# Kernel tuning notes

Measured on AMD Instinct MI355X. Metric: run time of the kernel, lower is better.

Reference implementation:

```python
import jax, jax.numpy as jnp
import numpy as np

D = 2048      # hidden_size
W = 4         # kernel_size
DG = 2048     # generator hidden size (no reduction)

def setup_inputs() -> dict:
    key = jax.random.key(0)
    k1, k2, k3, k4 = jax.random.split(key, 4)
    x = jax.random.normal(k1, (2, 4096, D), dtype=jnp.float32)
    # Linear weights stored torch-style [out, in]; scaled small for sane activations
    w1 = jax.random.normal(k2, (DG, D), dtype=jnp.float32) * 0.02
    w2 = jax.random.normal(k3, (D * W, DG), dtype=jnp.float32) * 0.02
    b2 = jax.random.normal(k4, (D * W,), dtype=jnp.float32) * 0.02
    return {"x": x, "w1": w1, "w2": w2, "b2": b2}

def reference(x, w1, w2, b2):
    B, T, Dh = x.shape
    # kernel generator: w2(silu(w1 @ x)) + b2 -> per-position kernels [B,T,D,W]
    h = jax.nn.silu(jnp.einsum('btd,gd->btg', x, w1))
    flat = jnp.einsum('btg,kg->btk', h, w2) + b2
    kernels = flat.reshape(B, T, Dh, W)
    # causal depthwise dynamic conv: y[b,t,d] = sum_w x[b, t-(W-1)+w, d] * k[b,t,d,w]
    xp = jnp.pad(x, ((0, 0), (W - 1, 0), (0, 0)))
    y = xp[:, 0:T, :] * kernels[..., 0]
    for w in range(1, W):  # small fixed-width loop over kernel taps
        y = y + xp[:, w:w + T, :] * kernels[..., w]
    return jax.nn.silu(y)
```

## Files before the change

kernel.cpp:

```cpp
#include <hip/hip_runtime.h>
#include <cstdint>

#define D_DIM  2048
#define T_DIM  4096
#define B_DIM  2
#define M_DIM  8192
#define DG_DIM 2048
#define N2_DIM 8192
#define K_DIM  2048
#define NT_TILES (K_DIM / 64)

typedef __bf16 bf16x8 __attribute__((ext_vector_type(8)));
typedef __bf16 bf16x4 __attribute__((ext_vector_type(4)));
typedef float  f32x4  __attribute__((ext_vector_type(4)));

__device__ __forceinline__ void gload_lds16(const void* g, void* l) {
  __builtin_amdgcn_global_load_lds(
      (__attribute__((address_space(1))) void*)g,
      (__attribute__((address_space(3))) void*)l, 16, 0, 0);
}

__device__ __forceinline__ float silu_f(float a) {
  return a / (1.f + __expf(-a));
}

__global__ void cast_f32_bf16(const float* __restrict__ src,
                              __bf16* __restrict__ dst, int n4) {
  int i = blockIdx.x * blockDim.x + threadIdx.x;
  if (i >= n4) return;
  float4 v = ((const float4*)src)[i];
  bf16x4 o;
  o[0] = (__bf16)v.x; o[1] = (__bf16)v.y; o[2] = (__bf16)v.z; o[3] = (__bf16)v.w;
  ((bf16x4*)dst)[i] = o;
}

__global__ void cast_permute_w2(const float* __restrict__ src,
                                __bf16* __restrict__ dst, int n4) {
  int i = blockIdx.x * blockDim.x + threadIdx.x;
  if (i >= n4) return;
  const int row = i >> 9;
  const int pos = i & 511;
  const int blk = row >> 8;
  const int cw  = row & 255;
  const int j   = cw >> 6;
  const int wn  = (cw >> 4) & 3;
  const int ln  = cw & 15;
  const int d   = blk * 64 + wn * 16 + ln;
  const int k   = 4 * d + j;
  float4 v = ((const float4*)src)[(size_t)k * 512 + pos];
  bf16x4 o;
  o[0] = (__bf16)v.x; o[1] = (__bf16)v.y; o[2] = (__bf16)v.z; o[3] = (__bf16)v.w;
  ((bf16x4*)dst)[i] = o;
}


__device__ __forceinline__ void stage_unit(const __bf16* src, __bf16* sX,
                                           int s, int hf, int lq0) {
  const int k0 = (s < NT_TILES) ? (s * 64) : 0;
  __bf16* dst = sX + ((s & 1) * 2 + hf) * 8192;
  const size_t goff = (size_t)hf * 128 * K_DIM + k0;
  gload_lds16(src + goff, dst + lq0);
  gload_lds16(src + goff + (size_t)64 * K_DIM, dst + lq0 + 4096);
}

__device__ __forceinline__ void read4(bf16x8 dst[4][2], const __bf16* base,
                                      const int off[4][2]) {
#pragma unroll
  for (int i = 0; i < 4; i++) {
    dst[i][0] = *(const bf16x8*)(base + off[i][0]);
    dst[i][1] = *(const bf16x8*)(base + off[i][1]);
  }
}

__device__ __forceinline__ void read2(bf16x8 dst[2][2], const __bf16* base,
                                      const int off[2][2]) {
#pragma unroll
  for (int j = 0; j < 2; j++) {
    dst[j][0] = *(const bf16x8*)(base + off[j][0]);
    dst[j][1] = *(const bf16x8*)(base + off[j][1]);
  }
}

__device__ __forceinline__ void mmaq(f32x4 acc[8][4], int ib, int jb,
                                     const bf16x8 a[4][2], const bf16x8 b[2][2]) {
  __builtin_amdgcn_s_setprio(1);
#pragma unroll
  for (int kk = 0; kk < 2; kk++)
#pragma unroll
    for (int i = 0; i < 4; i++)
#pragma unroll
      for (int j = 0; j < 2; j++)
        acc[ib + i][jb + j] = __builtin_amdgcn_mfma_f32_16x16x32_bf16(
            a[i][kk], b[j][kk], acc[ib + i][jb + j], 0, 0, 0);
  __builtin_amdgcn_s_setprio(0);
}

__device__ __forceinline__ void body_fn(f32x4 acc[8][4],
    bf16x8 aL[4][2], bf16x8 aH[4][2], bf16x8 b0[2][2], bf16x8 b1[2][2],
    const __bf16* nA, const __bf16* nB,
    const __bf16* a_src, const __bf16* b_src,
    __bf16* sA, __bf16* sB, int s2, int lq0,
    const int aoff[4][2], const int boff[2][2]) {
  mmaq(acc, 0, 0, aL, b0);
  __builtin_amdgcn_sched_barrier(0);
  stage_unit(a_src, sA, s2, 0, lq0);
  stage_unit(a_src, sA, s2, 1, lq0);
  stage_unit(b_src, sB, s2, 0, lq0);
  stage_unit(b_src, sB, s2, 1, lq0);
  __builtin_amdgcn_sched_barrier(0);
  mmaq(acc, 4, 0, aH, b0);
  __builtin_amdgcn_sched_barrier(0);
  read2(b0, nB, boff);
  __builtin_amdgcn_sched_barrier(0);
  mmaq(acc, 4, 2, aH, b1);
  __builtin_amdgcn_sched_barrier(0);
  read4(aH, nA + 8192, aoff);
  __builtin_amdgcn_sched_barrier(0);
  __builtin_amdgcn_s_setprio(1);
#pragma unroll
  for (int i = 0; i < 4; i++) {
#pragma unroll
    for (int kk = 0; kk < 2; kk++)
#pragma unroll
      for (int j = 0; j < 2; j++)
        acc[i][2 + j] = __builtin_amdgcn_mfma_f32_16x16x32_bf16(
            aL[i][kk], b1[j][kk], acc[i][2 + j], 0, 0, 0);
    aL[i][0] = *(const bf16x8*)(nA + aoff[i][0]);
    aL[i][1] = *(const bf16x8*)(nA + aoff[i][1]);
  }
  __builtin_amdgcn_s_setprio(0);
  __builtin_amdgcn_sched_barrier(0);
  read2(b1, nB + 8192, boff);
  asm volatile("s_waitcnt lgkmcnt(0)" ::: "memory");
  asm volatile("s_waitcnt vmcnt(0)" ::: "memory");
  __builtin_amdgcn_sched_barrier(0);
  __builtin_amdgcn_s_barrier();
  __builtin_amdgcn_sched_barrier(0);
}

__device__ __forceinline__ void gemm_core(const __bf16* __restrict__ A,
                                          const __bf16* __restrict__ B,
                                          int m0, int n0,
                                          __bf16* sA, __bf16* sB,
                                          f32x4 acc[8][4]) {
  constexpr int K = K_DIM;
  const int t    = threadIdx.x;
  const int lane = t & 63;
  const int wv   = t >> 6;
  const int wm   = wv >> 2;
  const int wn   = wv & 3;
  const int ln   = lane & 15, qd = lane >> 4;

  const __bf16 *a_src, *b_src;
  int lq0;
  {
    int q = t, row = q >> 3, cg = (q & 7) ^ (row & 7);
    a_src = A + (size_t)(m0 + row) * K + cg * 8;
    b_src = B + (size_t)(n0 + row) * K + cg * 8;
    lq0 = q * 8;
  }

  int aoff[4][2], boff[2][2];
#pragma unroll
  for (int i = 0; i < 4; i++)
#pragma unroll
    for (int kk = 0; kk < 2; kk++) {
      const int row = wm * 16 + i * 32 + ln;
      aoff[i][kk] = row * 64 + (((kk * 4 + qd) ^ (row & 7)) << 3);
    }
#pragma unroll
  for (int j = 0; j < 2; j++)
#pragma unroll
    for (int kk = 0; kk < 2; kk++) {
      const int row = j * 64 + wn * 16 + ln;
      boff[j][kk] = row * 64 + (((kk * 4 + qd) ^ (row & 7)) << 3);
    }

  const __bf16* A_p0 = sA;           const __bf16* A_p1 = sA + 16384;
  const __bf16* B_p0 = sB;           const __bf16* B_p1 = sB + 16384;

  bf16x8 aL[4][2], aH[4][2], b0[2][2], b1[2][2];

  stage_unit(a_src, sA, 0, 0, lq0);
  stage_unit(a_src, sA, 0, 1, lq0);
  stage_unit(b_src, sB, 0, 0, lq0);
  stage_unit(b_src, sB, 0, 1, lq0);
  stage_unit(a_src, sA, 1, 0, lq0);
  stage_unit(a_src, sA, 1, 1, lq0);
  stage_unit(b_src, sB, 1, 0, lq0);
  stage_unit(b_src, sB, 1, 1, lq0);
  asm volatile("s_waitcnt vmcnt(8)" ::: "memory");
  __builtin_amdgcn_s_barrier();
  __builtin_amdgcn_sched_barrier(0);
  read4(aL, A_p0, aoff);
  read4(aH, A_p0 + 8192, aoff);
  read2(b0, B_p0, boff);
  read2(b1, B_p0 + 8192, boff);
  asm volatile("s_waitcnt lgkmcnt(0)" ::: "memory");
  __builtin_amdgcn_sched_barrier(0);
  __builtin_amdgcn_s_barrier();
  __builtin_amdgcn_sched_barrier(0);

  for (int it = 0; it < NT_TILES / 2; ++it) {
    body_fn(acc, aL, aH, b0, b1, A_p1, B_p1, a_src, b_src, sA, sB,
            2 * it + 2, lq0, aoff, boff);
    body_fn(acc, aL, aH, b0, b1, A_p0, B_p0, a_src, b_src, sA, sB,
            2 * it + 3, lq0, aoff, boff);
  }
  asm volatile("s_waitcnt vmcnt(0)" ::: "memory");
}

__global__ __launch_bounds__(512) void gemm1_silu(
    const __bf16* __restrict__ A, const __bf16* __restrict__ B,
    __bf16* __restrict__ H) {
  __shared__ __bf16 sA[4 * 8192];
  __shared__ __bf16 sB[4 * 8192];
  const int m0 = blockIdx.y * 256, n0 = blockIdx.x * 256;
  f32x4 acc[8][4] = {};
  gemm_core(A, B, m0, n0, sA, sB, acc);

  const int lane = threadIdx.x & 63;
  const int wv   = threadIdx.x >> 6;
  const int wm   = wv >> 2, wn = wv & 3;
  const int ln   = lane & 15, qd = lane >> 4;
#pragma unroll
  for (int i = 0; i < 8; i++) {
    const int row0 = m0 + wm * 16 + i * 32 + qd * 4;
#pragma unroll
    for (int j = 0; j < 4; j++) {
      const int col = n0 + wn * 16 + j * 64 + ln;
#pragma unroll
      for (int r = 0; r < 4; r++)
        H[(size_t)(row0 + r) * DG_DIM + col] = (__bf16)silu_f(acc[i][j][r]);
    }
  }
}

__global__ __launch_bounds__(512) void gemm2_conv_silu(
    const __bf16* __restrict__ A, const __bf16* __restrict__ B,
    const float* __restrict__ b2, const float* __restrict__ x,
    float* __restrict__ out) {
  __shared__ __bf16 sA[4 * 8192];
  __shared__ __bf16 sB[4 * 8192];
  const int m0 = blockIdx.y * 256, n0 = blockIdx.x * 256;
  f32x4 acc[8][4] = {};
  gemm_core(A, B, m0, n0, sA, sB, acc);

  const int lane = threadIdx.x & 63;
  const int wv   = threadIdx.x >> 6;
  const int wm   = wv >> 2, wn = wv & 3;
  const int ln   = lane & 15, qd = lane >> 4;

  const int d = (n0 >> 2) + wn * 16 + ln;
  const float4 bias = *(const float4*)(b2 + 4 * d);

#pragma unroll
  for (int i = 0; i < 8; i++) {
    const int m_base = m0 + wm * 16 + i * 32 + qd * 4;
    const int b  = m_base >> 12;
    const int tb = m_base & 4095;
    float xv[7];
#pragma unroll
    for (int s = 0; s < 7; s++) {
      const int tp = tb + s - 3;
      xv[s] = (tp >= 0) ? x[((size_t)((b << 12) + tp)) * D_DIM + d] : 0.f;
    }
#pragma unroll
    for (int r = 0; r < 4; r++) {
      float y = (acc[i][0][r] + bias.x) * xv[r + 0]
              + (acc[i][1][r] + bias.y) * xv[r + 1]
              + (acc[i][2][r] + bias.z) * xv[r + 2]
              + (acc[i][3][r] + bias.w) * xv[r + 3];
      out[(size_t)(m_base + r) * D_DIM + d] = silu_f(y);
    }
  }
}

extern "C" void kernel_launch(void* const* d_in, const int* in_sizes, int n_in,
                              void* d_out, int out_size, void* d_ws, size_t ws_size,
                              hipStream_t stream) {
  (void)in_sizes; (void)n_in; (void)out_size; (void)ws_size;
  const float* x  = (const float*)d_in[0];
  const float* w1 = (const float*)d_in[1];
  const float* w2 = (const float*)d_in[2];
  const float* b2 = (const float*)d_in[3];
  float* out = (float*)d_out;

  __bf16* xb  = (__bf16*)d_ws;
  __bf16* w1b = xb  + (size_t)M_DIM * D_DIM;
  __bf16* w2b = w1b + (size_t)DG_DIM * D_DIM;
  __bf16* hb  = w2b + (size_t)N2_DIM * DG_DIM;

  {
    int n4 = M_DIM * D_DIM / 4;
    cast_f32_bf16<<<(n4 + 255) / 256, 256, 0, stream>>>(x, xb, n4);
  }
  {
    int n4 = DG_DIM * D_DIM / 4;
    cast_f32_bf16<<<(n4 + 255) / 256, 256, 0, stream>>>(w1, w1b, n4);
  }
  {
    int n4 = N2_DIM * DG_DIM / 4;
    cast_permute_w2<<<(n4 + 255) / 256, 256, 0, stream>>>(w2, w2b, n4);
  }

  gemm1_silu<<<dim3(DG_DIM / 256, M_DIM / 256), 512, 0, stream>>>(xb, w1b, hb);
  gemm2_conv_silu<<<dim3(N2_DIM / 256, M_DIM / 256), 512, 0, stream>>>(
      hb, w2b, b2, x, out);
}
```

Baseline: 469.5 us.

## Restructure GEMM main loop to load high halves lazily and move barrier mid-iteration

Reorders the per-tile schedule of the double-buffered MFMA loop. Each iteration now reads the high A/B fragments from the current LDS buffer at the start. It computes the low-A quadrants, waits and barriers mid-iteration, then issues the global-to-LDS staging. The high-A quadrants are computed while the next tile's low-A and B0 fragments are prefetched. The aim is to shorten register live ranges and to move the barrier and stall earlier, so staging overlaps more MFMA work. The risk is exposed LDS latency at the start of each tile and a changed overlap between staging and compute.

```diff
diff --git a/kernel.cpp b/kernel.cpp
--- a/kernel.cpp
+++ b/kernel.cpp
@@ -97,25 +97,27 @@
 
 __device__ __forceinline__ void body_fn(f32x4 acc[8][4],
     bf16x8 aL[4][2], bf16x8 aH[4][2], bf16x8 b0[2][2], bf16x8 b1[2][2],
-    const __bf16* nA, const __bf16* nB,
+    const __bf16* curA, const __bf16* curB,
+    const __bf16* nxtA, const __bf16* nxtB,
     const __bf16* a_src, const __bf16* b_src,
     __bf16* sA, __bf16* sB, int s2, int lq0,
     const int aoff[4][2], const int boff[2][2]) {
+  read2(b1, curB + 8192, boff);
+  read4(aH, curA + 8192, aoff);
+  __builtin_amdgcn_sched_barrier(0);
   mmaq(acc, 0, 0, aL, b0);
+  __builtin_amdgcn_sched_barrier(0);
+  mmaq(acc, 0, 2, aL, b1);
+  __builtin_amdgcn_sched_barrier(0);
+  asm volatile("s_waitcnt vmcnt(0) lgkmcnt(0)" ::: "memory");
+  __builtin_amdgcn_sched_barrier(0);
+  __builtin_amdgcn_s_barrier();
   __builtin_amdgcn_sched_barrier(0);
   stage_unit(a_src, sA, s2, 0, lq0);
   stage_unit(a_src, sA, s2, 1, lq0);
   stage_unit(b_src, sB, s2, 0, lq0);
   stage_unit(b_src, sB, s2, 1, lq0);
   __builtin_amdgcn_sched_barrier(0);
-  mmaq(acc, 4, 0, aH, b0);
-  __builtin_amdgcn_sched_barrier(0);
-  read2(b0, nB, boff);
-  __builtin_amdgcn_sched_barrier(0);
-  mmaq(acc, 4, 2, aH, b1);
-  __builtin_amdgcn_sched_barrier(0);
-  read4(aH, nA + 8192, aoff);
-  __builtin_amdgcn_sched_barrier(0);
   __builtin_amdgcn_s_setprio(1);
 #pragma unroll
   for (int i = 0; i < 4; i++) {
@@ -123,18 +125,28 @@
     for (int kk = 0; kk < 2; kk++)
 #pragma unroll
       for (int j = 0; j < 2; j++)
-        acc[i][2 + j] = __builtin_amdgcn_mfma_f32_16x16x32_bf16(
-            aL[i][kk], b1[j][kk], acc[i][2 + j], 0, 0, 0);
-    aL[i][0] = *(const bf16x8*)(nA + aoff[i][0]);
-    aL[i][1] = *(const bf16x8*)(nA + aoff[i][1]);
+        acc[4 + i][j] = __builtin_amdgcn_mfma_f32_16x16x32_bf16(
+            aH[i][kk], b0[j][kk], acc[4 + i][j], 0, 0, 0);
+    aL[i][0] = *(const bf16x8*)(nxtA + aoff[i][0]);
+    aL[i][1] = *(const bf16x8*)(nxtA + aoff[i][1]);
   }
   __builtin_amdgcn_s_setprio(0);
   __builtin_amdgcn_sched_barrier(0);
-  read2(b1, nB + 8192, boff);
-  asm volatile("s_waitcnt lgkmcnt(0)" ::: "memory");
-  asm volatile("s_waitcnt vmcnt(0)" ::: "memory");
-  __builtin_amdgcn_sched_barrier(0);
-  __builtin_amdgcn_s_barrier();
+  __builtin_amdgcn_s_setprio(1);
+#pragma unroll
+  for (int i = 0; i < 4; i++) {
+#pragma unroll
+    for (int kk = 0; kk < 2; kk++)
+#pragma unroll
+      for (int j = 0; j < 2; j++)
+        acc[4 + i][2 + j] = __builtin_amdgcn_mfma_f32_16x16x32_bf16(
+            aH[i][kk], b1[j][kk], acc[4 + i][2 + j], 0, 0, 0);
+    if (i < 2) {
+      b0[i][0] = *(const bf16x8*)(nxtB + boff[i][0]);
+      b0[i][1] = *(const bf16x8*)(nxtB + boff[i][1]);
+    }
+  }
+  __builtin_amdgcn_s_setprio(0);
   __builtin_amdgcn_sched_barrier(0);
 }
 
@@ -193,19 +205,14 @@
   __builtin_amdgcn_s_barrier();
   __builtin_amdgcn_sched_barrier(0);
   read4(aL, A_p0, aoff);
-  read4(aH, A_p0 + 8192, aoff);
   read2(b0, B_p0, boff);
-  read2(b1, B_p0 + 8192, boff);
-  asm volatile("s_waitcnt lgkmcnt(0)" ::: "memory");
-  __builtin_amdgcn_sched_barrier(0);
-  __builtin_amdgcn_s_barrier();
   __builtin_amdgcn_sched_barrier(0);
 
   for (int it = 0; it < NT_TILES / 2; ++it) {
-    body_fn(acc, aL, aH, b0, b1, A_p1, B_p1, a_src, b_src, sA, sB,
-            2 * it + 2, lq0, aoff, boff);
-    body_fn(acc, aL, aH, b0, b1, A_p0, B_p0, a_src, b_src, sA, sB,
-            2 * it + 3, lq0, aoff, boff);
+    body_fn(acc, aL, aH, b0, b1, A_p0, B_p0, A_p1, B_p1,
+            a_src, b_src, sA, sB, 2 * it + 2, lq0, aoff, boff);
+    body_fn(acc, aL, aH, b0, b1, A_p1, B_p1, A_p0, B_p0,
+            a_src, b_src, sA, sB, 2 * it + 3, lq0, aoff, boff);
   }
   asm volatile("s_waitcnt vmcnt(0)" ::: "memory");
 }
```

Result: slower. 481.5 us (+2.6%).
